# Kernel tuning notes

Measured on AMD Instinct MI355X. Metric: run time of the kernel, lower is better.

## Reference

```python
import jax, jax.numpy as jnp
import numpy as np

B, N, C = 4, 2048, 1024
H = 16
HD = C // H
SCALE = HD ** -0.5


def setup_inputs() -> dict:
    key = jax.random.key(0)
    ks = jax.random.split(key, 5)
    s = 0.02
    return {
        "x": jax.random.normal(ks[0], (B, N, C), dtype=jnp.float32),
        "w_qkv": jax.random.normal(ks[1], (C, 3 * C), dtype=jnp.float32) * s,
        "b_qkv": jnp.zeros((3 * C,), dtype=jnp.float32),
        "w_proj": jax.random.normal(ks[2], (C, C), dtype=jnp.float32) * s,
        "b_proj": jnp.zeros((C,), dtype=jnp.float32),
    }


def reference(x, w_qkv, b_qkv, w_proj, b_proj):
    b, n, c = x.shape
    qkv = x @ w_qkv + b_qkv                       # [b, n, 3c]
    qkv = qkv.reshape(b, n, 3, H, HD)
    qkv = jnp.transpose(qkv, (2, 0, 3, 1, 4))     # [3, b, h, n, hd]
    q, k, v = qkv[0], qkv[1], qkv[2]
    attn = jnp.einsum("bhqd,bhkd->bhqk", q, k) * SCALE
    attn = jax.nn.softmax(attn, axis=-1)
    out = jnp.einsum("bhqk,bhkd->bhqd", attn, v)  # [b, h, n, hd]
    out = jnp.transpose(out, (0, 2, 1, 3)).reshape(b, n, c)
    return out @ w_proj + b_proj
```

## Files before the change

kernel.cpp:

```cpp
#include <hip/hip_runtime.h>
#include <cstdint>
#include <cstddef>


typedef __attribute__((ext_vector_type(8))) short short8;
typedef __attribute__((ext_vector_type(4))) float f32x4;

#if __has_builtin(__builtin_amdgcn_exp2f)
#define EXP2F(x) __builtin_amdgcn_exp2f(x)
#else
#define EXP2F(x) __expf((x) * 0.69314718056f)
#endif

__device__ __forceinline__ short f2bf(float x) {
  unsigned u = __builtin_bit_cast(unsigned, x);
  u += 0x7fffu + ((u >> 16) & 1u);
  return (short)(u >> 16);
}

__device__ __forceinline__ void async16(const void* g, void* l) {
  __builtin_amdgcn_global_load_lds(
      (const __attribute__((address_space(1))) unsigned*)g,
      (__attribute__((address_space(3))) unsigned*)l, 16, 0, 0);
}


__global__ __launch_bounds__(256) void convert_kernel(const float* __restrict__ in,
                                                      short* __restrict__ out) {
  int i = blockIdx.x * 256 + threadIdx.x;
  const float4* p = (const float4*)in + (size_t)i * 2;
  float4 a = p[0], b = p[1];
  short8 r;
  r[0] = f2bf(a.x); r[1] = f2bf(a.y); r[2] = f2bf(a.z); r[3] = f2bf(a.w);
  r[4] = f2bf(b.x); r[5] = f2bf(b.y); r[6] = f2bf(b.z); r[7] = f2bf(b.w);
  *((short8*)out + i) = r;
}

__global__ __launch_bounds__(256) void wtrans_kernel(const float* __restrict__ in,
                                                     short* __restrict__ out,
                                                     int K, int N) {
  __shared__ float tile[32][33];
  int n0 = blockIdx.x * 32, k0 = blockIdx.y * 32;
  int tx = threadIdx.x, ty = threadIdx.y;
  for (int r = ty; r < 32; r += 8)
    tile[r][tx] = in[(size_t)(k0 + r) * N + n0 + tx];
  __syncthreads();
  for (int r = ty; r < 32; r += 8)
    out[(size_t)(n0 + r) * K + k0 + tx] = f2bf(tile[tx][r]);
}


template <int MODE>
__global__ __launch_bounds__(256) void gemm_kernel(
    const short* __restrict__ A, const short* __restrict__ Bt,
    const float* __restrict__ bias, int Nn,
    short* __restrict__ qb, short* __restrict__ kb, short* __restrict__ vtb,
    float* __restrict__ outp) {
  constexpr int K = 1024;
  __shared__ __align__(16) short As[128 * 32];
  __shared__ __align__(16) short Bs[128 * 32];
  const int tid = threadIdx.x, wave = tid >> 6, lane = tid & 63;
  const int quad = lane >> 4, l16 = lane & 15;
  const int m0 = blockIdx.y * 128, n0 = blockIdx.x * 128;
  const int wrow = (wave >> 1) * 64, wcol = (wave & 1) * 64;

  const int str = lane >> 2;
  const int sgc = ((lane & 3) ^ ((lane >> 3) & 3)) * 8;
  const short* Ag = A + (size_t)(m0 + str) * K + sgc;
  const short* Bg = Bt + (size_t)(n0 + str) * K + sgc;

  const int fsw = (l16 >> 1) & 3;

  f32x4 acc[4][4] = {};

  for (int k0 = 0; k0 < K; k0 += 32) {
#pragma unroll
    for (int i = 0; i < 2; ++i) {
      int c = wave * 2 + i;
      async16(Ag + (size_t)c * 16 * K + k0, (char*)As + c * 1024);
      async16(Bg + (size_t)c * 16 * K + k0, (char*)Bs + c * 1024);
    }
    __syncthreads();
    short8 af[4], bf[4];
#pragma unroll
    for (int t = 0; t < 4; ++t) {
      af[t] = *(const short8*)&As[(wrow + t * 16 + l16) * 32 + ((quad ^ fsw) << 3)];
      bf[t] = *(const short8*)&Bs[(wcol + t * 16 + l16) * 32 + ((quad ^ fsw) << 3)];
    }
#pragma unroll
    for (int mt = 0; mt < 4; ++mt)
#pragma unroll
      for (int nt = 0; nt < 4; ++nt)
        acc[mt][nt] = __builtin_amdgcn_mfma_f32_16x16x32_bf16(af[mt], bf[nt],
                                                              acc[mt][nt], 0, 0, 0);
    __syncthreads();
  }

  if (MODE == 0) {
#pragma unroll
    for (int mt = 0; mt < 4; ++mt) {
      int row0 = m0 + wrow + mt * 16 + quad * 4;
      int b = row0 >> 11, n = row0 & 2047;
#pragma unroll
      for (int nt = 0; nt < 4; ++nt) {
        int col = n0 + wcol + nt * 16 + l16;
        float bv = bias[col];
        float v0 = acc[mt][nt][0] + bv, v1 = acc[mt][nt][1] + bv;
        float v2 = acc[mt][nt][2] + bv, v3 = acc[mt][nt][3] + bv;
        int which = col >> 10;
        int h = (col >> 6) & 15;
        int d = col & 63;
        size_t bh = (size_t)(b * 16 + h);
        if (which == 0) {
          const float qs = 0.18033688f;
          size_t base = (bh * 2048 + n) * 64 + d;
          qb[base]       = f2bf(v0 * qs);
          qb[base + 64]  = f2bf(v1 * qs);
          qb[base + 128] = f2bf(v2 * qs);
          qb[base + 192] = f2bf(v3 * qs);
        } else if (which == 1) {
          size_t base = (bh * 2048 + n) * 64 + d;
          kb[base]       = f2bf(v0);
          kb[base + 64]  = f2bf(v1);
          kb[base + 128] = f2bf(v2);
          kb[base + 192] = f2bf(v3);
        } else {
          ushort4 pk;
          pk.x = (unsigned short)f2bf(v0);
          pk.y = (unsigned short)f2bf(v1);
          pk.z = (unsigned short)f2bf(v2);
          pk.w = (unsigned short)f2bf(v3);
          *(ushort4*)&vtb[(bh * 64 + d) * 2048 + n] = pk;
        }
      }
    }
  } else {
#pragma unroll
    for (int mt = 0; mt < 4; ++mt) {
      int row0 = m0 + wrow + mt * 16 + quad * 4;
#pragma unroll
      for (int nt = 0; nt < 4; ++nt) {
        int col = n0 + wcol + nt * 16 + l16;
        float bv = bias[col];
        outp[(size_t)row0 * Nn + col]       = acc[mt][nt][0] + bv;
        outp[(size_t)(row0 + 1) * Nn + col] = acc[mt][nt][1] + bv;
        outp[(size_t)(row0 + 2) * Nn + col] = acc[mt][nt][2] + bv;
        outp[(size_t)(row0 + 3) * Nn + col] = acc[mt][nt][3] + bv;
      }
    }
  }
}


__global__ __launch_bounds__(256) void attn_kernel(
    const short* __restrict__ qb, const short* __restrict__ kb,
    const short* __restrict__ vtb, short* __restrict__ ob) {
  __shared__ __align__(16) short Ks[2][64 * 64];
  __shared__ __align__(16) short Vs[2][64 * 64];
  __shared__ __align__(16) short Ps[4][32 * 64];
  __shared__ __align__(16) float Ls[4][32];
  const int tid = threadIdx.x, wave = tid >> 6, lane = tid & 63;
  const int quad = lane >> 4, l16 = lane & 15;
  const int q0 = blockIdx.x * 128;
  const int bh = blockIdx.y;
  const short* Qg = qb + (size_t)bh * (2048 * 64);
  const short* Kg = kb + (size_t)bh * (2048 * 64);
  const short* Vg = vtb + (size_t)bh * (64 * 2048);

  short8 qf[2][2];
#pragma unroll
  for (int qt = 0; qt < 2; ++qt)
#pragma unroll
    for (int kc = 0; kc < 2; ++kc)
      qf[qt][kc] = *(const short8*)
          &Qg[(size_t)(q0 + wave * 32 + qt * 16 + l16) * 64 + kc * 32 + quad * 8];

  const int str = lane >> 3;
  const int sgc = ((lane & 7) ^ (str & 7)) * 8;
  const int fsw = l16 & 7;
  short* Pw = Ps[wave];
  const int c0 = wave * 2, c1 = wave * 2 + 1;

  async16(Kg + (size_t)(c0 * 8 + str) * 64 + sgc, (char*)Ks[0] + c0 * 1024);
  async16(Kg + (size_t)(c1 * 8 + str) * 64 + sgc, (char*)Ks[0] + c1 * 1024);
  async16(Vg + (size_t)(c0 * 8 + str) * 2048 + sgc, (char*)Vs[0] + c0 * 1024);
  async16(Vg + (size_t)(c1 * 8 + str) * 2048 + sgc, (char*)Vs[0] + c1 * 1024);

  float lsum[2] = {0.f, 0.f};
  f32x4 oacc[2][4] = {};

#pragma unroll 2
  for (int t = 0; t < 32; ++t) {
    __syncthreads();

    int kvn = (t + 1) * 64;
    if (kvn < 2048) {
      char* kd = (char*)Ks[(t + 1) & 1];
      char* vd = (char*)Vs[(t + 1) & 1];
      async16(Kg + (size_t)(kvn + c0 * 8 + str) * 64 + sgc, kd + c0 * 1024);
      async16(Kg + (size_t)(kvn + c1 * 8 + str) * 64 + sgc, kd + c1 * 1024);
      async16(Vg + (size_t)(c0 * 8 + str) * 2048 + kvn + sgc, vd + c0 * 1024);
      async16(Vg + (size_t)(c1 * 8 + str) * 2048 + kvn + sgc, vd + c1 * 1024);
    }
    const short* Kst = Ks[t & 1];
    const short* Vst = Vs[t & 1];

    f32x4 sacc[2][4] = {};
#pragma unroll
    for (int kc = 0; kc < 2; ++kc) {
      short8 kf[4];
#pragma unroll
      for (int kvt = 0; kvt < 4; ++kvt)
        kf[kvt] = *(const short8*)
            &Kst[(kvt * 16 + l16) * 64 + (((kc * 4 + quad) ^ fsw) << 3)];
#pragma unroll
      for (int kvt = 0; kvt < 4; ++kvt)
#pragma unroll
        for (int qt = 0; qt < 2; ++qt)
          sacc[qt][kvt] = __builtin_amdgcn_mfma_f32_16x16x32_bf16(
              kf[kvt], qf[qt][kc], sacc[qt][kvt], 0, 0, 0);
    }

#pragma unroll
    for (int qt = 0; qt < 2; ++qt)
#pragma unroll
      for (int kvt = 0; kvt < 4; ++kvt) {
        float p0 = EXP2F(sacc[qt][kvt][0]);
        float p1 = EXP2F(sacc[qt][kvt][1]);
        float p2 = EXP2F(sacc[qt][kvt][2]);
        float p3 = EXP2F(sacc[qt][kvt][3]);
        lsum[qt] += (p0 + p1) + (p2 + p3);
        unsigned u0 = __builtin_bit_cast(unsigned, p0) + 0x8000u;
        unsigned u1 = __builtin_bit_cast(unsigned, p1) + 0x8000u;
        unsigned u2 = __builtin_bit_cast(unsigned, p2) + 0x8000u;
        unsigned u3 = __builtin_bit_cast(unsigned, p3) + 0x8000u;
        uint2 w;
        w.x = (u0 >> 16) | (u1 & 0xffff0000u);
        w.y = (u2 >> 16) | (u3 & 0xffff0000u);
        *(uint2*)&Pw[(qt * 16 + l16) * 64 +
                     ((((kvt * 2 + (quad >> 1)) ^ fsw)) << 3) + (quad & 1) * 4] = w;
      }

    __asm__ volatile("s_waitcnt lgkmcnt(0)" ::: "memory");

#pragma unroll
    for (int kc = 0; kc < 2; ++kc) {
      short8 pf[2], vf[4];
#pragma unroll
      for (int qt = 0; qt < 2; ++qt)
        pf[qt] = *(const short8*)
            &Pw[(qt * 16 + l16) * 64 + (((kc * 4 + quad) ^ fsw) << 3)];
#pragma unroll
      for (int nt = 0; nt < 4; ++nt)
        vf[nt] = *(const short8*)
            &Vst[(nt * 16 + l16) * 64 + (((kc * 4 + quad) ^ fsw) << 3)];
#pragma unroll
      for (int qt = 0; qt < 2; ++qt)
#pragma unroll
        for (int nt = 0; nt < 4; ++nt)
          oacc[qt][nt] = __builtin_amdgcn_mfma_f32_16x16x32_bf16(
              pf[qt], vf[nt], oacc[qt][nt], 0, 0, 0);
    }
  }

#pragma unroll
  for (int qt = 0; qt < 2; ++qt) {
    float v = lsum[qt];
    v += __shfl_xor(v, 16, 64);
    v += __shfl_xor(v, 32, 64);
    if (quad == 0) Ls[wave][qt * 16 + l16] = v;
  }
  __asm__ volatile("s_waitcnt lgkmcnt(0)" ::: "memory");

  const int b = bh >> 4, h = bh & 15;
#pragma unroll
  for (int qt = 0; qt < 2; ++qt) {
    float4 lr = *(const float4*)&Ls[wave][qt * 16 + quad * 4];
    float inv0 = 1.f / lr.x, inv1 = 1.f / lr.y, inv2 = 1.f / lr.z, inv3 = 1.f / lr.w;
#pragma unroll
    for (int nt = 0; nt < 4; ++nt) {
      int d = nt * 16 + l16;
      int qbase = q0 + wave * 32 + qt * 16 + quad * 4;
      size_t obase = ((size_t)(b * 2048 + qbase)) * 1024 + h * 64 + d;
      ob[obase]        = f2bf(oacc[qt][nt][0] * inv0);
      ob[obase + 1024] = f2bf(oacc[qt][nt][1] * inv1);
      ob[obase + 2048] = f2bf(oacc[qt][nt][2] * inv2);
      ob[obase + 3072] = f2bf(oacc[qt][nt][3] * inv3);
    }
  }
}


extern "C" void kernel_launch(void* const* d_in, const int* in_sizes, int n_in,
                              void* d_out, int out_size, void* d_ws, size_t ws_size,
                              hipStream_t stream) {
  const float* x      = (const float*)d_in[0];
  const float* w_qkv  = (const float*)d_in[1];
  const float* b_qkv  = (const float*)d_in[2];
  const float* w_proj = (const float*)d_in[3];
  const float* b_proj = (const float*)d_in[4];
  float* out = (float*)d_out;

  short* xs     = (short*)d_ws;
  short* wqkvT  = xs + (size_t)8192 * 1024;
  short* wprojT = wqkvT + (size_t)3072 * 1024;
  short* qb     = wprojT + (size_t)1024 * 1024;
  short* kb     = qb + (size_t)64 * 2048 * 64;
  short* vtb    = kb + (size_t)64 * 2048 * 64;
  short* aob    = vtb + (size_t)64 * 2048 * 64;

  convert_kernel<<<dim3(4096), 256, 0, stream>>>(x, xs);
  wtrans_kernel<<<dim3(96, 32), dim3(32, 8), 0, stream>>>(w_qkv, wqkvT, 1024, 3072);
  wtrans_kernel<<<dim3(32, 32), dim3(32, 8), 0, stream>>>(w_proj, wprojT, 1024, 1024);

  gemm_kernel<0><<<dim3(24, 64), 256, 0, stream>>>(xs, wqkvT, b_qkv, 3072,
                                                   qb, kb, vtb, nullptr);
  attn_kernel<<<dim3(16, 64), 256, 0, stream>>>(qb, kb, vtb, aob);
  gemm_kernel<1><<<dim3(8, 64), 256, 0, stream>>>(aob, wprojT, b_proj, 1024,
                                                  nullptr, nullptr, nullptr, out);
}
```

Before: 307.1 us.

## Load V directly from global in fp16, drop V LDS staging

The attention kernel no longer stages V tiles through shared memory. Each wave loads its V fragments straight from global memory into registers, with V and P stored as fp16 via packed round-toward-zero conversion, and the PV product uses the f16 MFMA. Launch bounds now request 4 blocks per SM and the loop unroll pragma is removed. This frees LDS and cuts LDS traffic, but adds uncached-style global loads whose latency sits inside the loop, and it changes the numeric precision of P and V.

```diff
diff --git a/kernel.cpp b/kernel.cpp
--- a/kernel.cpp
+++ b/kernel.cpp
@@ -5,6 +5,7 @@
 
 typedef __attribute__((ext_vector_type(8))) short short8;
 typedef __attribute__((ext_vector_type(4))) float f32x4;
+typedef _Float16 half8 __attribute__((ext_vector_type(8)));
 
 #if __has_builtin(__builtin_amdgcn_exp2f)
 #define EXP2F(x) __builtin_amdgcn_exp2f(x)
@@ -16,6 +17,11 @@
   unsigned u = __builtin_bit_cast(unsigned, x);
   u += 0x7fffu + ((u >> 16) & 1u);
   return (short)(u >> 16);
+}
+
+__device__ __forceinline__ unsigned pkh(float a, float b) {
+  auto h = __builtin_amdgcn_cvt_pkrtz(a, b);
+  return __builtin_bit_cast(unsigned, h);
 }
 
 __device__ __forceinline__ void async16(const void* g, void* l) {
@@ -125,12 +131,10 @@
           kb[base + 128] = f2bf(v2);
           kb[base + 192] = f2bf(v3);
         } else {
-          ushort4 pk;
-          pk.x = (unsigned short)f2bf(v0);
-          pk.y = (unsigned short)f2bf(v1);
-          pk.z = (unsigned short)f2bf(v2);
-          pk.w = (unsigned short)f2bf(v3);
-          *(ushort4*)&vtb[(bh * 64 + d) * 2048 + n] = pk;
+          uint2 pk;
+          pk.x = pkh(v0, v1);
+          pk.y = pkh(v2, v3);
+          *(uint2*)&vtb[(bh * 64 + d) * 2048 + n] = pk;
         }
       }
     }
@@ -152,11 +156,10 @@
 }
 
 
-__global__ __launch_bounds__(256) void attn_kernel(
+__global__ __launch_bounds__(256, 4) void attn_kernel(
     const short* __restrict__ qb, const short* __restrict__ kb,
     const short* __restrict__ vtb, short* __restrict__ ob) {
   __shared__ __align__(16) short Ks[2][64 * 64];
-  __shared__ __align__(16) short Vs[2][64 * 64];
   __shared__ __align__(16) short Ps[4][32 * 64];
   __shared__ __align__(16) float Ls[4][32];
   const int tid = threadIdx.x, wave = tid >> 6, lane = tid & 63;
@@ -165,7 +168,7 @@
   const int bh = blockIdx.y;
   const short* Qg = qb + (size_t)bh * (2048 * 64);
   const short* Kg = kb + (size_t)bh * (2048 * 64);
-  const short* Vg = vtb + (size_t)bh * (64 * 2048);
+  const _Float16* Vg = (const _Float16*)(vtb + (size_t)bh * (64 * 2048));
 
   short8 qf[2][2];
 #pragma unroll
@@ -183,27 +186,21 @@
 
   async16(Kg + (size_t)(c0 * 8 + str) * 64 + sgc, (char*)Ks[0] + c0 * 1024);
   async16(Kg + (size_t)(c1 * 8 + str) * 64 + sgc, (char*)Ks[0] + c1 * 1024);
-  async16(Vg + (size_t)(c0 * 8 + str) * 2048 + sgc, (char*)Vs[0] + c0 * 1024);
-  async16(Vg + (size_t)(c1 * 8 + str) * 2048 + sgc, (char*)Vs[0] + c1 * 1024);
 
   float lsum[2] = {0.f, 0.f};
   f32x4 oacc[2][4] = {};
 
-#pragma unroll 2
   for (int t = 0; t < 32; ++t) {
     __syncthreads();
 
     int kvn = (t + 1) * 64;
     if (kvn < 2048) {
       char* kd = (char*)Ks[(t + 1) & 1];
-      char* vd = (char*)Vs[(t + 1) & 1];
       async16(Kg + (size_t)(kvn + c0 * 8 + str) * 64 + sgc, kd + c0 * 1024);
       async16(Kg + (size_t)(kvn + c1 * 8 + str) * 64 + sgc, kd + c1 * 1024);
-      async16(Vg + (size_t)(c0 * 8 + str) * 2048 + kvn + sgc, vd + c0 * 1024);
-      async16(Vg + (size_t)(c1 * 8 + str) * 2048 + kvn + sgc, vd + c1 * 1024);
     }
     const short* Kst = Ks[t & 1];
-    const short* Vst = Vs[t & 1];
+    const int kv0 = t * 64;
 
     f32x4 sacc[2][4] = {};
 #pragma unroll
@@ -220,6 +217,14 @@
           sacc[qt][kvt] = __builtin_amdgcn_mfma_f32_16x16x32_bf16(
               kf[kvt], qf[qt][kc], sacc[qt][kvt], 0, 0, 0);
     }
+
+    half8 vf[2][4];
+#pragma unroll
+    for (int kc = 0; kc < 2; ++kc)
+#pragma unroll
+      for (int nt = 0; nt < 4; ++nt)
+        vf[kc][nt] = *(const half8*)
+            &Vg[(size_t)(nt * 16 + l16) * 2048 + kv0 + kc * 32 + quad * 8];
 
 #pragma unroll
     for (int qt = 0; qt < 2; ++qt)
@@ -230,13 +235,9 @@
         float p2 = EXP2F(sacc[qt][kvt][2]);
         float p3 = EXP2F(sacc[qt][kvt][3]);
         lsum[qt] += (p0 + p1) + (p2 + p3);
-        unsigned u0 = __builtin_bit_cast(unsigned, p0) + 0x8000u;
-        unsigned u1 = __builtin_bit_cast(unsigned, p1) + 0x8000u;
-        unsigned u2 = __builtin_bit_cast(unsigned, p2) + 0x8000u;
-        unsigned u3 = __builtin_bit_cast(unsigned, p3) + 0x8000u;
         uint2 w;
-        w.x = (u0 >> 16) | (u1 & 0xffff0000u);
-        w.y = (u2 >> 16) | (u3 & 0xffff0000u);
+        w.x = pkh(p0, p1);
+        w.y = pkh(p2, p3);
         *(uint2*)&Pw[(qt * 16 + l16) * 64 +
                      ((((kvt * 2 + (quad >> 1)) ^ fsw)) << 3) + (quad & 1) * 4] = w;
       }
@@ -245,21 +246,17 @@
 
 #pragma unroll
     for (int kc = 0; kc < 2; ++kc) {
-      short8 pf[2], vf[4];
+      half8 pf[2];
 #pragma unroll
       for (int qt = 0; qt < 2; ++qt)
-        pf[qt] = *(const short8*)
-            &Pw[(qt * 16 + l16) * 64 + (((kc * 4 + quad) ^ fsw) << 3)];
-#pragma unroll
-      for (int nt = 0; nt < 4; ++nt)
-        vf[nt] = *(const short8*)
-            &Vst[(nt * 16 + l16) * 64 + (((kc * 4 + quad) ^ fsw) << 3)];
+        pf[qt] = __builtin_bit_cast(half8, *(const short8*)
+            &Pw[(qt * 16 + l16) * 64 + (((kc * 4 + quad) ^ fsw) << 3)]);
 #pragma unroll
       for (int qt = 0; qt < 2; ++qt)
 #pragma unroll
         for (int nt = 0; nt < 4; ++nt)
-          oacc[qt][nt] = __builtin_amdgcn_mfma_f32_16x16x32_bf16(
-              pf[qt], vf[nt], oacc[qt][nt], 0, 0, 0);
+          oacc[qt][nt] = __builtin_amdgcn_mfma_f32_16x16x32_f16(
+              pf[qt], vf[kc][nt], oacc[qt][nt], 0, 0, 0);
     }
   }
 
```

Result: slower. 443.2 us (+44.3%).
